# Performance work log

Measured on AMD Instinct MI355X. Metric: run time of the kernel, lower is better.

Reference implementation:

```python
import jax, jax.numpy as jnp
import numpy as np

C = 512
NUM_HEADS = 8


def setup_inputs() -> dict:
    key = jax.random.key(0)
    ks = jax.random.split(key, 9)
    s = 1.0 / np.sqrt(C)
    inp = {
        "x": jax.random.normal(ks[0], (2, C, 64, 64), dtype=jnp.float32),
        "Wq": jax.random.uniform(ks[1], (C, C), jnp.float32, -s, s),
        "bq": jax.random.uniform(ks[2], (C,), jnp.float32, -s, s),
        "Wk": jax.random.uniform(ks[3], (C, C), jnp.float32, -s, s),
        "bk": jax.random.uniform(ks[4], (C,), jnp.float32, -s, s),
        "Wv": jax.random.uniform(ks[5], (C, C), jnp.float32, -s, s),
        "bv": jax.random.uniform(ks[6], (C,), jnp.float32, -s, s),
        "Wp": jax.random.uniform(ks[7], (C, C), jnp.float32, -s, s),
        "bp": jax.random.uniform(ks[8], (C,), jnp.float32, -s, s),
    }
    return inp


def _split_heads(t):
    # [B, S, C] -> [B, h, S, d]
    B, S, Ct = t.shape
    return t.reshape(B, S, NUM_HEADS, Ct // NUM_HEADS).transpose(0, 2, 1, 3)


def reference(x, Wq, bq, Wk, bk, Wv, bv, Wp, bp):
    B, Ct, H, W = x.shape
    tok = x.transpose(0, 2, 3, 1).reshape(B, H * W, Ct)  # [B, S, C]
    q = _split_heads(tok @ Wq.T + bq)
    k = _split_heads(tok @ Wk.T + bk)
    v = _split_heads(tok @ Wv.T + bv)
    d = q.shape[-1]
    scores = jnp.einsum("bhsd,bhtd->bhst", q, k) / jnp.sqrt(jnp.float32(d))
    attn = jax.nn.softmax(scores, axis=-1)
    out = jnp.einsum("bhst,bhtd->bhsd", attn, v)
    out = out.transpose(0, 2, 1, 3).reshape(B, H * W, Ct)  # merge heads
    out = out @ Wp.T + bp
    return out.reshape(B, H, W, Ct).transpose(0, 3, 1, 2)
```

## Files before the change

### kernel.cpp

```cpp
#include <hip/hip_runtime.h>
#include <stdint.h>
#include <math.h>

typedef unsigned short u16;
typedef uint32_t u32;
typedef short bf16x8 __attribute__((ext_vector_type(8)));
typedef float f32x4  __attribute__((ext_vector_type(4)));

#define DEV __device__ __forceinline__

DEV u16 f2bf(float f) {
    union { float f; u32 u; } x; x.f = f;
    u32 lsb = (x.u >> 16) & 1u;
    x.u += 0x7fffu + lsb;
    return (u16)(x.u >> 16);
}

DEV u32 pack2(float a, float b) {
    union { float f; u32 u; } x, y; x.f = a; y.f = b;
    return __builtin_amdgcn_perm(y.u + 0x8000u, x.u + 0x8000u, 0x07060302u);
}

#if __has_builtin(__builtin_amdgcn_exp2f)
DEV float fexp2(float x) { return __builtin_amdgcn_exp2f(x); }
#else
DEV float fexp2(float x) { return __expf(x * 0.69314718056f); }
#endif

DEV f32x4 mfma16(bf16x8 a, bf16x8 b, f32x4 c) {
    return __builtin_amdgcn_mfma_f32_16x16x32_bf16(a, b, c, 0, 0, 0);
}

__global__ __launch_bounds__(256) void convert_w_kernel(const float* __restrict__ w0,
                                                        const float* __restrict__ w1,
                                                        const float* __restrict__ w2,
                                                        const float* __restrict__ w3,
                                                        u16* __restrict__ dst) {
    const float* src = (blockIdx.y == 0) ? w0 : (blockIdx.y == 1) ? w1
                     : (blockIdx.y == 2) ? w2 : w3;
    int idx = (blockIdx.x * 256 + threadIdx.x) * 4;
    float4 v = *(const float4*)&src[idx];
    uint2 pv;
    pv.x = pack2(v.x, v.y);
    pv.y = pack2(v.z, v.w);
    *(uint2*)&dst[(size_t)blockIdx.y * 262144 + idx] = pv;
}

__global__ __launch_bounds__(256) void transpose_kernel(const float* __restrict__ x,
                                                        u16* __restrict__ tok) {
    __shared__ u16 t[64][65];
    const int b = blockIdx.z, c0 = blockIdx.y * 64, s0 = blockIdx.x * 64;
    const float* xb = x + ((size_t)b * 512 + c0) * 4096 + s0;
    u16* tb = tok + ((size_t)b * 4096 + s0) * 512 + c0;
    const int tid = threadIdx.x;
    {
        const int jc = tid & 15, i0 = tid >> 4;
#pragma unroll
        for (int ii = 0; ii < 4; ii++) {
            int i = i0 * 4 + ii;
            float4 v = *(const float4*)&xb[(size_t)i * 4096 + jc * 4];
            t[i][jc * 4 + 0] = f2bf(v.x);
            t[i][jc * 4 + 1] = f2bf(v.y);
            t[i][jc * 4 + 2] = f2bf(v.z);
            t[i][jc * 4 + 3] = f2bf(v.w);
        }
    }
    __syncthreads();
    {
        const int j = tid & 31, i0 = tid >> 5;
#pragma unroll
        for (int ii = 0; ii < 8; ii++) {
            int srow = i0 * 8 + ii;
            u32 v = (u32)t[j * 2][srow] | ((u32)t[j * 2 + 1][srow] << 16);
            *(u32*)(&tb[(size_t)srow * 512 + j * 2]) = v;
        }
    }
}

DEV void proj_core(const u16* __restrict__ W, const float* __restrict__ bias,
                   const u16* __restrict__ Bb, void* __restrict__ out,
                   int b, int mode, float scale,
                   u16 (*__restrict__ Alds)[4096], u16 (*__restrict__ Blds)[4096]) {
    const int tid = threadIdx.x;
    const int wave = tid >> 6, lane = tid & 63, q = lane >> 4, c = lane & 15;
    const int m0 = blockIdx.y * 128, n0 = blockIdx.x * 128;

    const int cs = tid & 15, qs = (tid >> 4) & 3, ms = (tid >> 6) & 3;
    const u16* Asrc0 = W  + (size_t)(m0 + ms * 16 + cs) * 512 + qs * 8;
    const u16* Asrc1 = W  + (size_t)(m0 + (ms + 4) * 16 + cs) * 512 + qs * 8;
    const u16* Bsrc0 = Bb + (size_t)(n0 + ms * 16 + cs) * 512 + qs * 8;
    const u16* Bsrc1 = Bb + (size_t)(n0 + (ms + 4) * 16 + cs) * 512 + qs * 8;

    f32x4 acc[4][4] = {};

    *(int4*)&Alds[0][tid * 8]         = *(const int4*)&Asrc0[0];
    *(int4*)&Alds[0][(tid + 256) * 8] = *(const int4*)&Asrc1[0];
    *(int4*)&Blds[0][tid * 8]         = *(const int4*)&Bsrc0[0];
    *(int4*)&Blds[0][(tid + 256) * 8] = *(const int4*)&Bsrc1[0];
    __syncthreads();

    for (int it = 0; it < 16; it++) {
        const int p = it & 1;
        const int kn = ((it + 1) & 15) * 32;

        int4 ast0 = *(const int4*)&Asrc0[kn];
        int4 ast1 = *(const int4*)&Asrc1[kn];
        int4 bst0 = *(const int4*)&Bsrc0[kn];
        int4 bst1 = *(const int4*)&Bsrc1[kn];

        bf16x8 af[4], bfr[4];
#pragma unroll
        for (int t = 0; t < 4; t++) {
            int gm = (((wave & 1) * 4 + t) * 4 + q) * 16 + c;
            af[t] = *(const bf16x8*)&Alds[p][gm * 8];
            int gn = (((wave >> 1) * 4 + t) * 4 + q) * 16 + c;
            bfr[t] = *(const bf16x8*)&Blds[p][gn * 8];
        }
#pragma unroll
        for (int mt = 0; mt < 4; mt++)
#pragma unroll
            for (int nt = 0; nt < 4; nt++)
                acc[mt][nt] = mfma16(af[mt], bfr[nt], acc[mt][nt]);

        *(int4*)&Alds[1 - p][tid * 8]         = ast0;
        *(int4*)&Alds[1 - p][(tid + 256) * 8] = ast1;
        *(int4*)&Blds[1 - p][tid * 8]         = bst0;
        *(int4*)&Blds[1 - p][(tid + 256) * 8] = bst1;
        __syncthreads();
    }

    const int mbase = m0 + (wave & 1) * 64, nbase = n0 + (wave >> 1) * 64;
#pragma unroll
    for (int mt = 0; mt < 4; mt++) {
        int co0 = mbase + mt * 16 + q * 4;
        float b0 = bias[co0 + 0], b1 = bias[co0 + 1];
        float b2 = bias[co0 + 2], b3 = bias[co0 + 3];
#pragma unroll
        for (int nt = 0; nt < 4; nt++) {
            int scol = nbase + nt * 16 + c;
            float v0 = (acc[mt][nt][0] + b0) * scale;
            float v1 = (acc[mt][nt][1] + b1) * scale;
            float v2 = (acc[mt][nt][2] + b2) * scale;
            float v3 = (acc[mt][nt][3] + b3) * scale;
            if (mode == 0) {
                uint2 pv; pv.x = pack2(v0, v1); pv.y = pack2(v2, v3);
                size_t idx = ((size_t)(b * 8 + (co0 >> 6)) * 4096 + scol) * 64 + (co0 & 63);
                *(uint2*)&((u16*)out)[idx] = pv;
            } else if (mode == 1) {
                u16* o = (u16*)out;
                o[((size_t)(b * 512 + co0 + 0)) * 4096 + scol] = f2bf(v0);
                o[((size_t)(b * 512 + co0 + 1)) * 4096 + scol] = f2bf(v1);
                o[((size_t)(b * 512 + co0 + 2)) * 4096 + scol] = f2bf(v2);
                o[((size_t)(b * 512 + co0 + 3)) * 4096 + scol] = f2bf(v3);
            } else {
                float* o = (float*)out;
                o[((size_t)(b * 512 + co0 + 0)) * 4096 + scol] = v0;
                o[((size_t)(b * 512 + co0 + 1)) * 4096 + scol] = v1;
                o[((size_t)(b * 512 + co0 + 2)) * 4096 + scol] = v2;
                o[((size_t)(b * 512 + co0 + 3)) * 4096 + scol] = v3;
            }
        }
    }
}

__global__ __launch_bounds__(256) void qkv_kernel(const u16* __restrict__ Wbf,
                                                  const float* __restrict__ bq,
                                                  const float* __restrict__ bk,
                                                  const float* __restrict__ bv,
                                                  const u16* __restrict__ tok,
                                                  u16* __restrict__ Qb,
                                                  u16* __restrict__ Kb,
                                                  u16* __restrict__ Vb) {
    __shared__ u16 Alds[2][4096];
    __shared__ u16 Blds[2][4096];
    const int z = blockIdx.z, j = z >> 1, b = z & 1;
    const u16* W = Wbf + (size_t)j * 262144;
    const float* bias = (j == 0) ? bq : (j == 1) ? bk : bv;
    void* out = (j == 0) ? (void*)Qb : (j == 1) ? (void*)Kb : (void*)Vb;
    const float scale = (j == 0) ? 0.1803368801f : 1.0f;
    const int mode = (j == 2) ? 1 : 0;
    proj_core(W, bias, tok + (size_t)b * (4096 * 512), out, b, mode, scale, Alds, Blds);
}

__global__ __launch_bounds__(256) void projp_kernel(const u16* __restrict__ Wp,
                                                    const float* __restrict__ bp,
                                                    const u16* __restrict__ attout,
                                                    float* __restrict__ out) {
    __shared__ u16 Alds[2][4096];
    __shared__ u16 Blds[2][4096];
    const int b = blockIdx.z;
    proj_core(Wp, bp, attout + (size_t)b * (4096 * 512), out, b, 2, 1.0f, Alds, Blds);
}

__global__ __launch_bounds__(256) void attn_kernel(const u16* __restrict__ Qm,
                                                   const u16* __restrict__ Km,
                                                   const u16* __restrict__ Vm,
                                                   u16* __restrict__ attout) {
    __shared__ u16 Klds[2][4096];
    __shared__ u16 Vlds[2][4096];
    __shared__ u16 Plds[128 * 72];
    const int tid = threadIdx.x, wave = tid >> 6, lane = tid & 63;
    const int q = lane >> 4, c = lane & 15;
    const int bhd = blockIdx.y, s0 = blockIdx.x * 128;
    const u16* Qb = Qm + (size_t)bhd * (4096 * 64);
    const u16* Kb = Km + (size_t)bhd * (4096 * 64);
    const u16* Vb = Vm + (size_t)bhd * (64 * 4096);

    bf16x8 qf[2][2];
#pragma unroll
    for (int st = 0; st < 2; st++)
#pragma unroll
        for (int kd = 0; kd < 2; kd++)
            qf[st][kd] = *(const bf16x8*)
                &Qb[(size_t)(s0 + wave * 32 + st * 16 + c) * 64 + kd * 32 + q * 8];

    const int rr = tid & 15, qq = (tid >> 4) & 3, kk = (tid >> 6) & 1;
    const int t40 = tid >> 7, t41 = t40 + 2;
    const u16* Ksrc0 = Kb + (size_t)(t40 * 16 + rr) * 64 + kk * 32 + qq * 8;
    const u16* Ksrc1 = Kb + (size_t)(t41 * 16 + rr) * 64 + kk * 32 + qq * 8;
    const u16* Vsrc0 = Vb + (size_t)(t40 * 16 + rr) * 4096 + kk * 32 + qq * 8;
    const u16* Vsrc1 = Vb + (size_t)(t41 * 16 + rr) * 4096 + kk * 32 + qq * 8;
    u16* Prow = &Plds[(size_t)(wave * 32 + c) * 72];

    f32x4 oacc[4][2] = {};
    float lsum[2] = {0.f, 0.f};

    *(int4*)&Klds[0][tid * 8]         = *(const int4*)&Ksrc0[0];
    *(int4*)&Klds[0][(tid + 256) * 8] = *(const int4*)&Ksrc1[0];
    *(int4*)&Vlds[0][tid * 8]         = *(const int4*)&Vsrc0[0];
    *(int4*)&Vlds[0][(tid + 256) * 8] = *(const int4*)&Vsrc1[0];
    __syncthreads();

    for (int it = 0; it < 64; it++) {
        const int p = it & 1;
        const size_t t0n = (size_t)(((it + 1) & 63) * 64);

        int4 kst0 = *(const int4*)&Ksrc0[t0n * 64];
        int4 kst1 = *(const int4*)&Ksrc1[t0n * 64];
        int4 vst0 = *(const int4*)&Vsrc0[t0n];
        int4 vst1 = *(const int4*)&Vsrc1[t0n];

        f32x4 sacc[4][2] = {};
#pragma unroll
        for (int kd = 0; kd < 2; kd++) {
            bf16x8 ka[4];
#pragma unroll
            for (int tt = 0; tt < 4; tt++)
                ka[tt] = *(const bf16x8*)&Klds[p][(((tt * 2 + kd) * 4 + q) * 16 + c) * 8];
#pragma unroll
            for (int tt = 0; tt < 4; tt++)
#pragma unroll
                for (int st = 0; st < 2; st++)
                    sacc[tt][st] = mfma16(ka[tt], qf[st][kd], sacc[tt][st]);
        }

#pragma unroll
        for (int st = 0; st < 2; st++) {
#pragma unroll
            for (int tt = 0; tt < 4; tt++) {
                float p0 = fexp2(sacc[tt][st][0]);
                float p1 = fexp2(sacc[tt][st][1]);
                float p2 = fexp2(sacc[tt][st][2]);
                float p3 = fexp2(sacc[tt][st][3]);
                lsum[st] += (p0 + p1) + (p2 + p3);
                uint2 pv; pv.x = pack2(p0, p1); pv.y = pack2(p2, p3);
                *(uint2*)&Prow[st * (16 * 72) + tt * 16 + q * 4] = pv;
            }
        }

#pragma unroll
        for (int kt = 0; kt < 2; kt++) {
            bf16x8 va[4], pb[2];
#pragma unroll
            for (int dt = 0; dt < 4; dt++)
                va[dt] = *(const bf16x8*)&Vlds[p][(((dt * 2 + kt) * 4 + q) * 16 + c) * 8];
#pragma unroll
            for (int st = 0; st < 2; st++)
                pb[st] = *(const bf16x8*)&Prow[st * (16 * 72) + kt * 32 + q * 8];
#pragma unroll
            for (int dt = 0; dt < 4; dt++)
#pragma unroll
                for (int st = 0; st < 2; st++)
                    oacc[dt][st] = mfma16(va[dt], pb[st], oacc[dt][st]);
        }

        *(int4*)&Klds[1 - p][tid * 8]         = kst0;
        *(int4*)&Klds[1 - p][(tid + 256) * 8] = kst1;
        *(int4*)&Vlds[1 - p][tid * 8]         = vst0;
        *(int4*)&Vlds[1 - p][(tid + 256) * 8] = vst1;
        __syncthreads();
    }

    const int b = bhd >> 3, hd = bhd & 7;
#pragma unroll
    for (int st = 0; st < 2; st++) {
        float l = lsum[st];
        l += __shfl_xor(l, 16, 64);
        l += __shfl_xor(l, 32, 64);
        float rl = 1.0f / l;
        int s = s0 + wave * 32 + st * 16 + c;
#pragma unroll
        for (int dt = 0; dt < 4; dt++) {
            uint2 pv;
            pv.x = pack2(oacc[dt][st][0] * rl, oacc[dt][st][1] * rl);
            pv.y = pack2(oacc[dt][st][2] * rl, oacc[dt][st][3] * rl);
            size_t idx = ((size_t)(b * 4096 + s)) * 512 + hd * 64 + dt * 16 + q * 4;
            *(uint2*)&attout[idx] = pv;
        }
    }
}

extern "C" void kernel_launch(void* const* d_in, const int* in_sizes, int n_in,
                              void* d_out, int out_size, void* d_ws, size_t ws_size,
                              hipStream_t stream) {
    (void)in_sizes; (void)n_in; (void)out_size; (void)ws_size;
    const float* x  = (const float*)d_in[0];
    const float* Wq = (const float*)d_in[1];
    const float* bq = (const float*)d_in[2];
    const float* Wk = (const float*)d_in[3];
    const float* bk = (const float*)d_in[4];
    const float* Wv = (const float*)d_in[5];
    const float* bv = (const float*)d_in[6];
    const float* Wp = (const float*)d_in[7];
    const float* bp = (const float*)d_in[8];
    float* out = (float*)d_out;

    const size_t NTOK = (size_t)4 * 1024 * 1024;
    u16* tok = (u16*)d_ws;
    u16* Qb  = tok + NTOK;
    u16* Kb  = Qb + NTOK;
    u16* Vb  = Kb + NTOK;
    u16* Wbf = Vb + NTOK;
    u16* attout = tok;

    convert_w_kernel<<<dim3(256, 4), 256, 0, stream>>>(Wq, Wk, Wv, Wp, Wbf);
    transpose_kernel<<<dim3(64, 8, 2), 256, 0, stream>>>(x, tok);
    qkv_kernel<<<dim3(32, 4, 6), 256, 0, stream>>>(Wbf, bq, bk, bv, tok, Qb, Kb, Vb);
    attn_kernel<<<dim3(32, 16), 256, 0, stream>>>(Qb, Kb, Vb, attout);
    projp_kernel<<<dim3(32, 4, 2), 256, 0, stream>>>(Wbf + 3 * 262144, bp, attout, out);
}
```

Baseline: 232.9 us.

## Merge weight conversion into transpose kernel and deepen GEMM prefetch to three stages

```diff
diff --git a/kernel.cpp b/kernel.cpp
--- a/kernel.cpp
+++ b/kernel.cpp
@@ -31,49 +31,51 @@
     return __builtin_amdgcn_mfma_f32_16x16x32_bf16(a, b, c, 0, 0, 0);
 }
 
-__global__ __launch_bounds__(256) void convert_w_kernel(const float* __restrict__ w0,
-                                                        const float* __restrict__ w1,
-                                                        const float* __restrict__ w2,
-                                                        const float* __restrict__ w3,
-                                                        u16* __restrict__ dst) {
-    const float* src = (blockIdx.y == 0) ? w0 : (blockIdx.y == 1) ? w1
-                     : (blockIdx.y == 2) ? w2 : w3;
-    int idx = (blockIdx.x * 256 + threadIdx.x) * 4;
-    float4 v = *(const float4*)&src[idx];
-    uint2 pv;
-    pv.x = pack2(v.x, v.y);
-    pv.y = pack2(v.z, v.w);
-    *(uint2*)&dst[(size_t)blockIdx.y * 262144 + idx] = pv;
-}
-
-__global__ __launch_bounds__(256) void transpose_kernel(const float* __restrict__ x,
-                                                        u16* __restrict__ tok) {
+__global__ __launch_bounds__(256) void prep_kernel(const float* __restrict__ x,
+                                                   u16* __restrict__ tok,
+                                                   const float* __restrict__ w0,
+                                                   const float* __restrict__ w1,
+                                                   const float* __restrict__ w2,
+                                                   const float* __restrict__ w3,
+                                                   u16* __restrict__ dst) {
     __shared__ u16 t[64][65];
-    const int b = blockIdx.z, c0 = blockIdx.y * 64, s0 = blockIdx.x * 64;
-    const float* xb = x + ((size_t)b * 512 + c0) * 4096 + s0;
-    u16* tb = tok + ((size_t)b * 4096 + s0) * 512 + c0;
-    const int tid = threadIdx.x;
-    {
-        const int jc = tid & 15, i0 = tid >> 4;
-#pragma unroll
-        for (int ii = 0; ii < 4; ii++) {
-            int i = i0 * 4 + ii;
-            float4 v = *(const float4*)&xb[(size_t)i * 4096 + jc * 4];
-            t[i][jc * 4 + 0] = f2bf(v.x);
-            t[i][jc * 4 + 1] = f2bf(v.y);
-            t[i][jc * 4 + 2] = f2bf(v.z);
-            t[i][jc * 4 + 3] = f2bf(v.w);
-        }
-    }
-    __syncthreads();
-    {
-        const int j = tid & 31, i0 = tid >> 5;
-#pragma unroll
-        for (int ii = 0; ii < 8; ii++) {
-            int srow = i0 * 8 + ii;
-            u32 v = (u32)t[j * 2][srow] | ((u32)t[j * 2 + 1][srow] << 16);
-            *(u32*)(&tb[(size_t)srow * 512 + j * 2]) = v;
-        }
+    const int id = blockIdx.x, tid = threadIdx.x;
+    if (id < 1024) {
+        const int b = id >> 9, c0 = ((id >> 6) & 7) * 64, s0 = (id & 63) * 64;
+        const float* xb = x + ((size_t)b * 512 + c0) * 4096 + s0;
+        u16* tb = tok + ((size_t)b * 4096 + s0) * 512 + c0;
+        {
+            const int jc = tid & 15, i0 = tid >> 4;
+#pragma unroll
+            for (int ii = 0; ii < 4; ii++) {
+                int i = i0 * 4 + ii;
+                float4 v = *(const float4*)&xb[(size_t)i * 4096 + jc * 4];
+                t[i][jc * 4 + 0] = f2bf(v.x);
+                t[i][jc * 4 + 1] = f2bf(v.y);
+                t[i][jc * 4 + 2] = f2bf(v.z);
+                t[i][jc * 4 + 3] = f2bf(v.w);
+            }
+        }
+        __syncthreads();
+        {
+            const int j = tid & 31, i0 = tid >> 5;
+#pragma unroll
+            for (int ii = 0; ii < 8; ii++) {
+                int srow = i0 * 8 + ii;
+                u32 v = (u32)t[j * 2][srow] | ((u32)t[j * 2 + 1][srow] << 16);
+                *(u32*)(&tb[(size_t)srow * 512 + j * 2]) = v;
+            }
+        }
+    } else {
+        const int id2 = id - 1024;
+        const int j = id2 >> 8;
+        const float* src = (j == 0) ? w0 : (j == 1) ? w1 : (j == 2) ? w2 : w3;
+        int idx = ((id2 & 255) * 256 + tid) * 4;
+        float4 v = *(const float4*)&src[idx];
+        uint2 pv;
+        pv.x = pack2(v.x, v.y);
+        pv.y = pack2(v.z, v.w);
+        *(uint2*)&dst[(size_t)j * 262144 + idx] = pv;
     }
 }
 
@@ -93,20 +95,28 @@
 
     f32x4 acc[4][4] = {};
 
-    *(int4*)&Alds[0][tid * 8]         = *(const int4*)&Asrc0[0];
-    *(int4*)&Alds[0][(tid + 256) * 8] = *(const int4*)&Asrc1[0];
-    *(int4*)&Blds[0][tid * 8]         = *(const int4*)&Bsrc0[0];
-    *(int4*)&Blds[0][(tid + 256) * 8] = *(const int4*)&Bsrc1[0];
+    int4 pa0 = *(const int4*)&Asrc0[0];
+    int4 pa1 = *(const int4*)&Asrc1[0];
+    int4 pb0 = *(const int4*)&Bsrc0[0];
+    int4 pb1 = *(const int4*)&Bsrc1[0];
+    int4 ha0 = *(const int4*)&Asrc0[32];
+    int4 ha1 = *(const int4*)&Asrc1[32];
+    int4 hb0 = *(const int4*)&Bsrc0[32];
+    int4 hb1 = *(const int4*)&Bsrc1[32];
+    *(int4*)&Alds[0][tid * 8]         = pa0;
+    *(int4*)&Alds[0][(tid + 256) * 8] = pa1;
+    *(int4*)&Blds[0][tid * 8]         = pb0;
+    *(int4*)&Blds[0][(tid + 256) * 8] = pb1;
     __syncthreads();
 
+    int p = 0, pw = 1;
     for (int it = 0; it < 16; it++) {
-        const int p = it & 1;
-        const int kn = ((it + 1) & 15) * 32;
-
-        int4 ast0 = *(const int4*)&Asrc0[kn];
-        int4 ast1 = *(const int4*)&Asrc1[kn];
-        int4 bst0 = *(const int4*)&Bsrc0[kn];
-        int4 bst1 = *(const int4*)&Bsrc1[kn];
+        const int kn = ((it + 2) & 15) * 32;
+
+        int4 na0 = *(const int4*)&Asrc0[kn];
+        int4 na1 = *(const int4*)&Asrc1[kn];
+        int4 nb0 = *(const int4*)&Bsrc0[kn];
+        int4 nb1 = *(const int4*)&Bsrc1[kn];
 
         bf16x8 af[4], bfr[4];
 #pragma unroll
@@ -122,11 +132,13 @@
             for (int nt = 0; nt < 4; nt++)
                 acc[mt][nt] = mfma16(af[mt], bfr[nt], acc[mt][nt]);
 
-        *(int4*)&Alds[1 - p][tid * 8]         = ast0;
-        *(int4*)&Alds[1 - p][(tid + 256) * 8] = ast1;
-        *(int4*)&Blds[1 - p][tid * 8]         = bst0;
-        *(int4*)&Blds[1 - p][(tid + 256) * 8] = bst1;
+        *(int4*)&Alds[pw][tid * 8]         = ha0;
+        *(int4*)&Alds[pw][(tid + 256) * 8] = ha1;
+        *(int4*)&Blds[pw][tid * 8]         = hb0;
+        *(int4*)&Blds[pw][(tid + 256) * 8] = hb1;
+        ha0 = na0; ha1 = na1; hb0 = nb0; hb1 = nb1;
         __syncthreads();
+        p = pw; pw = (pw == 2) ? 0 : pw + 1;
     }
 
     const int mbase = m0 + (wave & 1) * 64, nbase = n0 + (wave >> 1) * 64;
@@ -171,8 +183,8 @@
                                                   u16* __restrict__ Qb,
                                                   u16* __restrict__ Kb,
                                                   u16* __restrict__ Vb) {
-    __shared__ u16 Alds[2][4096];
-    __shared__ u16 Blds[2][4096];
+    __shared__ u16 Alds[3][4096];
+    __shared__ u16 Blds[3][4096];
     const int z = blockIdx.z, j = z >> 1, b = z & 1;
     const u16* W = Wbf + (size_t)j * 262144;
     const float* bias = (j == 0) ? bq : (j == 1) ? bk : bv;
@@ -186,8 +198,8 @@
                                                     const float* __restrict__ bp,
                                                     const u16* __restrict__ attout,
                                                     float* __restrict__ out) {
-    __shared__ u16 Alds[2][4096];
-    __shared__ u16 Blds[2][4096];
+    __shared__ u16 Alds[3][4096];
+    __shared__ u16 Blds[3][4096];
     const int b = blockIdx.z;
     proj_core(Wp, bp, attout + (size_t)b * (4096 * 512), out, b, 2, 1.0f, Alds, Blds);
 }
@@ -333,8 +345,7 @@
     u16* Wbf = Vb + NTOK;
     u16* attout = tok;
 
-    convert_w_kernel<<<dim3(256, 4), 256, 0, stream>>>(Wq, Wk, Wv, Wp, Wbf);
-    transpose_kernel<<<dim3(64, 8, 2), 256, 0, stream>>>(x, tok);
+    prep_kernel<<<dim3(2048), 256, 0, stream>>>(x, tok, Wq, Wk, Wv, Wp, Wbf);
     qkv_kernel<<<dim3(32, 4, 6), 256, 0, stream>>>(Wbf, bq, bk, bv, tok, Qb, Kb, Vb);
     attn_kernel<<<dim3(32, 16), 256, 0, stream>>>(Qb, Kb, Vb, attout);
     projp_kernel<<<dim3(32, 4, 2), 256, 0, stream>>>(Wbf + 3 * 262144, bp, attout, out);
```

Measured after the change: 224.4 us. 3.7% less time.
